# Performance work log

Measured on AMD Instinct MI355X. Metric: run time of the kernel, lower is better.

The kernel has to match this reference:

```python
import jax, jax.numpy as jnp
import numpy as np

B, N, V, E, T = 32, 256, 16, 1024, 5
MAX_N, ANNO, ND, VD, A_ACT = 256, 18, 64, 64, 3


def position_encoding_init(n_position, emb_dim):
    pe = np.array([[pos / np.power(10000, 2 * (j // 2) / emb_dim) for j in range(emb_dim)]
                   if pos != 0 else np.zeros(emb_dim) for pos in range(n_position)])
    pe[1:, 0::2] = np.sin(pe[1:, 0::2])
    pe[1:, 1::2] = np.cos(pe[1:, 1::2])
    return jnp.asarray(pe, jnp.float32)


def gru_cell(x, h, Wih, Whh, bih=None, bhh=None):
    # PyTorch GRUCell semantics. Wih: [3H, in], Whh: [3H, H]
    gi = x @ Wih.T + (bih if bih is not None else 0.0)
    gh = h @ Whh.T + (bhh if bhh is not None else 0.0)
    i_r, i_z, i_n = jnp.split(gi, 3, axis=1)
    h_r, h_z, h_n = jnp.split(gh, 3, axis=1)
    r = jax.nn.sigmoid(i_r + h_r)
    z = jax.nn.sigmoid(i_z + h_z)
    n = jnp.tanh(i_n + r * h_n)
    return (1.0 - z) * n + z * h


def setup_inputs() -> dict:
    key = jax.random.key(0)
    ks = jax.random.split(key, 20)
    dec_in = E + ND + 2 * VD
    inp = {
        "annotation": jax.random.normal(ks[0], (B, N, ANNO), jnp.float32),
        "A_out": jax.random.bernoulli(ks[1], 0.05, (B, N, N)).astype(jnp.float32),
        "A_in": jax.random.bernoulli(ks[2], 0.05, (B, N, N)).astype(jnp.float32),
        "from_node": jax.random.randint(ks[3], (B,), 0, MAX_N),
        "vnf_now": jax.random.uniform(ks[4], (B, V), jnp.float32),
        "vnf_all": jax.random.uniform(ks[5], (B, V), jnp.float32),
        "mask": jax.random.randint(ks[6], (B * N,), 0, 2),
        "anno_W": jax.random.normal(ks[7], (ANNO, E), jnp.float32),
        "gru_Wih": jax.random.normal(ks[8], (3 * E, 2 * E), jnp.float32) / np.sqrt(2 * E),
        "gru_Whh": jax.random.normal(ks[9], (3 * E, E), jnp.float32) / np.sqrt(E),
        "vnf_now_W": jax.random.normal(ks[10], (V, VD), jnp.float32),
        "vnf_all_W": jax.random.normal(ks[11], (V, VD), jnp.float32),
        "dgru_Wih": jax.random.normal(ks[12], (6 * E, dec_in), jnp.float32) / np.sqrt(dec_in),
        "dgru_Whh": jax.random.normal(ks[13], (6 * E, 2 * E), jnp.float32) / np.sqrt(2 * E),
        "dgru_bih": jax.random.normal(ks[14], (6 * E,), jnp.float32) * 0.01,
        "dgru_bhh": jax.random.normal(ks[15], (6 * E,), jnp.float32) * 0.01,
        "out_W1": jax.random.normal(ks[16], (E, 2 * E), jnp.float32) / np.sqrt(2 * E),
        "out_b1": jnp.zeros((E,), jnp.float32),
        "out_W2": jax.random.normal(ks[17], (A_ACT, E), jnp.float32) / np.sqrt(E),
        "out_b2": jnp.zeros((A_ACT,), jnp.float32),
        "pos_enc": position_encoding_init(MAX_N, ND),
    }
    return inp


def reference(annotation, A_out, A_in, from_node, vnf_now, vnf_all, mask,
              anno_W, gru_Wih, gru_Whh, vnf_now_W, vnf_all_W,
              dgru_Wih, dgru_Whh, dgru_bih, dgru_bhh,
              out_W1, out_b1, out_W2, out_b2, pos_enc):
    BN = B * N
    # ---- encoder (GG-NN): block-diagonal adjacency matmul == batched matmul ----
    h = annotation.reshape(BN, ANNO) @ anno_W  # [BN, E]

    def step(h, _):
        hb = h.reshape(B, N, E)
        a_out = jnp.einsum('bnm,bme->bne', A_out, hb).reshape(BN, E)
        a_in = jnp.einsum('bnm,bme->bne', A_in, hb).reshape(BN, E)
        a = jnp.concatenate([a_out, a_in], axis=1)  # [BN, 2E]
        return gru_cell(a, h, gru_Wih, gru_Whh), None

    enc_out, _ = jax.lax.scan(step, h, None, length=T)  # [BN, E]

    # ---- decoder step ----
    vn = (vnf_now @ vnf_now_W)[:, None, :]  # [B,1,VD] (repeat over N)
    va = (vnf_all @ vnf_all_W)[:, None, :]
    npos = pos_enc[from_node][:, None, :]   # [B,1,ND]
    vn = jnp.broadcast_to(vn, (B, N, VD)).reshape(BN, VD)
    va = jnp.broadcast_to(va, (B, N, VD)).reshape(BN, VD)
    npos = jnp.broadcast_to(npos, (B, N, ND)).reshape(BN, ND)

    concat_input = jnp.concatenate([enc_out, npos, va, vn], axis=1)
    h0 = jnp.zeros((BN, 2 * E), jnp.float32)
    hidden = gru_cell(concat_input, h0, dgru_Wih, dgru_Whh, dgru_bih, dgru_bhh)

    mid = jax.nn.relu(hidden @ out_W1.T + out_b1)
    output = (mid @ out_W2.T + out_b2).reshape(B, N, A_ACT)

    max_v = jnp.max(output, axis=(1, 2), keepdims=True)  # [B,1,1]
    output = output - (max_v + 1.0)
    mask_f = jnp.where(mask == 1, 1.0, 1e10).astype(jnp.float32).reshape(B, N, 1)
    output = mask_f * output + 1.0

    node_logits = output[:, :, 0]            # [B, N]
    vnf_logits = output[:, :, 1:]            # [B, N, 2]
    return node_logits, vnf_logits, hidden
```

## Files before the change

### kernel.cpp

```cpp
#include <hip/hip_runtime.h>
#include <hip/hip_bf16.h>
#include <math.h>

#define B_ 32
#define N_ 256
#define E_ 1024
#define BN_ 8192

typedef __hip_bfloat16 bf16;
typedef __bf16 bf8v __attribute__((ext_vector_type(8)));
typedef float  f4v  __attribute__((ext_vector_type(4)));

__device__ __forceinline__ float b2f(bf16 v) {
    unsigned short u = *(unsigned short*)&v;
    return __uint_as_float(((unsigned)u) << 16);
}
__device__ __forceinline__ unsigned short f2bu(float f) {
    bf16 h = __float2bfloat16(f);
    return *(unsigned short*)&h;
}
__device__ __forceinline__ float4 load4bf(const bf16* p) {
    ushort4 u = *(const ushort4*)p;
    return make_float4(__uint_as_float((unsigned)u.x << 16),
                       __uint_as_float((unsigned)u.y << 16),
                       __uint_as_float((unsigned)u.z << 16),
                       __uint_as_float((unsigned)u.w << 16));
}
__device__ __forceinline__ void store4bf(bf16* p, float a, float b, float c, float d) {
    ushort4 u = make_ushort4(f2bu(a), f2bu(b), f2bu(c), f2bu(d));
    *(ushort4*)p = u;
}
__device__ __forceinline__ float safe_sigm(float x) {
    x = fminf(fmaxf(x, -40.0f), 40.0f);
    return 1.0f / (1.0f + expf(-x));
}
__device__ __forceinline__ float safe_tanh(float x) {
    x = fminf(fmaxf(x, -15.0f), 15.0f);
    float t = expf(2.0f * x);
    return (t - 1.0f) / (t + 1.0f);
}
__device__ __forceinline__ void glds16(const bf16* g, bf16* l) {
    __builtin_amdgcn_global_load_lds(
        (__attribute__((address_space(1))) const void*)g,
        (__attribute__((address_space(3))) void*)l, 16, 0, 0);
}

#define MFMA16(d, a, b) d = __builtin_amdgcn_mfma_f32_16x16x32_bf16(a, b, d, 0, 0, 0)

__global__ __launch_bounds__(256)
void w2bf_kernel(const float* __restrict__ src, bf16* __restrict__ dst, int n4)
{
    int i = blockIdx.x * 256 + threadIdx.x;
    if (i < n4) {
        float4 v = ((const float4*)src)[i];
        store4bf(dst + (size_t)i * 4, v.x, v.y, v.z, v.w);
    }
}

__global__ __launch_bounds__(256)
void wgpack_kernel(const float* __restrict__ Wih, const float* __restrict__ Whh,
                   bf16* __restrict__ Wg)
{
    const int wr = blockIdx.x;
    const int e16 = wr / 48, rem = wr % 48;
    const int gate = rem >> 4, eL = rem & 15;
    const int e = e16 * 16 + eL;
    const float* s1 = Wih + (size_t)(gate * 1024 + e) * 2048;
    const float* s2 = Whh + (size_t)(gate * 1024 + e) * 1024;
    bf16* d = Wg + (size_t)wr * 3072;
    const int k0 = threadIdx.x * 4;
#pragma unroll
    for (int rep = 0; rep < 2; ++rep) {
        int k = k0 + rep * 1024;
        float4 v = *(const float4*)(s1 + k);
        store4bf(d + k, v.x, v.y, v.z, v.w);
    }
    {
        float4 v = *(const float4*)(s2 + k0);
        store4bf(d + 2048 + k0, v.x, v.y, v.z, v.w);
    }
}

__global__ __launch_bounds__(256)
void dgpack_kernel(const float* __restrict__ Wih, bf16* __restrict__ Wg)
{
    const int wr = blockIdx.x;
    const int e16 = wr / 48, rem = wr % 48;
    const int gate = rem >> 4, eL = rem & 15;
    const int e = e16 * 16 + eL;
    const float* s = Wih + (size_t)(gate * 2048 + e) * 1216;
    bf16* d = Wg + (size_t)wr * 1216;
    for (int k4 = threadIdx.x; k4 < 304; k4 += 256) {
        float4 v = *(const float4*)(s + k4 * 4);
        store4bf(d + k4 * 4, v.x, v.y, v.z, v.w);
    }
}

__global__ __launch_bounds__(256)
void anno_kernel(const float* __restrict__ anno, const float* __restrict__ W,
                 bf16* __restrict__ Hb)
{
    __shared__ float s[18];
    int row = blockIdx.x;
    if (threadIdx.x < 18) s[threadIdx.x] = anno[row * 18 + threadIdx.x];
    __syncthreads();
    for (int j = threadIdx.x; j < 1024; j += 256) {
        float acc = 0.0f;
#pragma unroll
        for (int k = 0; k < 18; ++k) acc = fmaf(s[k], W[k * 1024 + j], acc);
        Hb[(size_t)row * 1024 + j] = __float2bfloat16(acc);
    }
}

__global__ __launch_bounds__(256)
void bmm_kernel(const float* __restrict__ Aout, const float* __restrict__ Ain,
                const bf16* __restrict__ H, bf16* __restrict__ Abuf)
{
    __shared__ float As[16][68];
    __shared__ float Bs[16][68];
    const int z = blockIdx.z;
    const int b = z >> 1, which = z & 1;
    const float* Amat = (which ? Ain : Aout) + (size_t)b * N_ * N_;
    const bf16* Bmat = H + (size_t)b * N_ * E_;
    const int t = threadIdx.x;
    const int tx = t & 15, ty = t >> 4;
    const int bm = blockIdx.x * 64;
    const int bn = blockIdx.y * 64;
    const int ar = t >> 2, ak = (t & 3) << 2;
    const int kr = t >> 4, kn = (t & 15) << 2;
    float acc[4][4] = {};
    for (int k0 = 0; k0 < N_; k0 += 16) {
        float4 av = *(const float4*)(Amat + (size_t)(bm + ar) * N_ + k0 + ak);
        As[ak + 0][ar] = av.x; As[ak + 1][ar] = av.y;
        As[ak + 2][ar] = av.z; As[ak + 3][ar] = av.w;
        float4 bv = load4bf(Bmat + (size_t)(k0 + kr) * E_ + bn + kn);
        *(float4*)&Bs[kr][kn] = bv;
        __syncthreads();
#pragma unroll
        for (int kk = 0; kk < 16; ++kk) {
            float4 a4 = *(const float4*)&As[kk][ty << 2];
            float4 b4 = *(const float4*)&Bs[kk][tx << 2];
            float am[4] = {a4.x, a4.y, a4.z, a4.w};
            float bb[4] = {b4.x, b4.y, b4.z, b4.w};
#pragma unroll
            for (int i = 0; i < 4; ++i)
#pragma unroll
                for (int j = 0; j < 4; ++j)
                    acc[i][j] = fmaf(am[i], bb[j], acc[i][j]);
        }
        __syncthreads();
    }
#pragma unroll
    for (int i = 0; i < 4; ++i) {
        int row = b * N_ + bm + (ty << 2) + i;
        int col = which * 1024 + bn + (tx << 2);
        store4bf(&Abuf[(size_t)row * 2048 + col], acc[i][0], acc[i][1], acc[i][2], acc[i][3]);
    }
}

__global__ __launch_bounds__(256)
void htrans_kernel(const bf16* __restrict__ H, bf16* __restrict__ HbT)
{
    __shared__ float s[64][65];
    const int b = blockIdx.z;
    const int e0 = blockIdx.x * 64;
    const int n0 = blockIdx.y * 64;
    const bf16* Hb = H + (size_t)b * N_ * E_;
    bf16* Tb = HbT + (size_t)b * E_ * N_;
    const int t = threadIdx.x;
    const int tr = t >> 4, tc = (t & 15) << 2;
#pragma unroll
    for (int i = 0; i < 4; ++i) {
        float4 v = load4bf(Hb + (size_t)(n0 + tr + i * 16) * E_ + e0 + tc);
        s[tr + i * 16][tc + 0] = v.x; s[tr + i * 16][tc + 1] = v.y;
        s[tr + i * 16][tc + 2] = v.z; s[tr + i * 16][tc + 3] = v.w;
    }
    __syncthreads();
#pragma unroll
    for (int i = 0; i < 4; ++i) {
        int e = tr + i * 16;
        store4bf(Tb + (size_t)(e0 + e) * N_ + n0 + tc,
                 s[tc + 0][e], s[tc + 1][e], s[tc + 2][e], s[tc + 3][e]);
    }
}

__global__ __launch_bounds__(256)
void bmm_mfma_kernel(const bf16* __restrict__ Aoutb, const bf16* __restrict__ Ainb,
                     const bf16* __restrict__ HbT, bf16* __restrict__ Abuf)
{
    __shared__ bf16 As[64 * 32];
    __shared__ bf16 Bs[64 * 32];
    const int t = threadIdx.x;
    const int lane = t & 63, w = t >> 6;
    const int wm = (w >> 1) * 32, wn = (w & 1) * 32;
    const int z = blockIdx.z, b = z >> 1, which = z & 1;
    const int bm = blockIdx.x * 64, bn = blockIdx.y * 64;
    const int quad = lane >> 4, fr = lane & 15;
    const int srow = t >> 2, slot = t & 3;
    const int g = (slot + ((srow >> 1) & 3)) & 3;
    const int lds_off = srow * 32 + slot * 8;

    f4v acc[2][2];
#pragma unroll
    for (int i = 0; i < 2; ++i)
#pragma unroll
        for (int j = 0; j < 2; ++j) acc[i][j] = (f4v){0.f, 0.f, 0.f, 0.f};

    int aoff[2], boff[2];
#pragma unroll
    for (int i = 0; i < 2; ++i) {
        int arow = wm + 16 * i + fr;
        int s = (quad - ((arow >> 1) & 3)) & 3;
        aoff[i] = arow * 32 + s * 8;
    }
#pragma unroll
    for (int j = 0; j < 2; ++j) {
        int n = wn + 16 * j + fr;
        int s = (quad - ((n >> 1) & 3)) & 3;
        boff[j] = n * 32 + s * 8;
    }

    const bf16* Ap = (which ? Ainb : Aoutb) + (size_t)b * N_ * N_
                   + (size_t)(bm + srow) * N_ + g * 8;
    const bf16* Bp = HbT + (size_t)b * E_ * N_ + (size_t)(bn + srow) * N_ + g * 8;
    for (int k0 = 0; k0 < N_; k0 += 32) {
        float4 av = *(const float4*)(Ap + k0);
        float4 bv4 = *(const float4*)(Bp + k0);
        __syncthreads();
        *(float4*)(As + lds_off) = av;
        *(float4*)(Bs + lds_off) = bv4;
        __syncthreads();
        bf8v af0 = *(const bf8v*)(As + aoff[0]);
        bf8v af1 = *(const bf8v*)(As + aoff[1]);
#pragma unroll
        for (int j = 0; j < 2; ++j) {
            bf8v bv = *(const bf8v*)(Bs + boff[j]);
            MFMA16(acc[0][j], af0, bv);
            MFMA16(acc[1][j], af1, bv);
        }
    }
#pragma unroll
    for (int i = 0; i < 2; ++i)
#pragma unroll
        for (int j = 0; j < 2; ++j)
#pragma unroll
            for (int r = 0; r < 4; ++r) {
                int row = b * N_ + bm + wm + 16 * i + quad * 4 + r;
                int col = which * 1024 + bn + wn + 16 * j + fr;
                Abuf[(size_t)row * 2048 + col] = __float2bfloat16(acc[i][j][r]);
            }
}

__global__ __launch_bounds__(256, 2)
void enc_gru_kernel(const bf16* __restrict__ Aab, const bf16* __restrict__ Wg,
                    const bf16* __restrict__ Hcur, bf16* __restrict__ Hnext)
{
    __shared__ __align__(16) bf16 As[2 * 128 * 32];
    __shared__ __align__(16) bf16 Bs[2 * 192 * 32];
    const int t = threadIdx.x;
    const int lane = t & 63, w = t >> 6;
    const int wm = (w >> 1) * 64;
    const int wnH = (w & 1);
    const int bm = blockIdx.x * 128;
    const int bY = blockIdx.y;
    const int quad = lane >> 4, fr = lane & 15;

    f4v ar[2][4], az[2][4], ani[2][4], anh[2][4];
#pragma unroll
    for (int gq = 0; gq < 2; ++gq)
#pragma unroll
        for (int i = 0; i < 4; ++i) {
            ar[gq][i] = (f4v){0.f, 0.f, 0.f, 0.f};
            az[gq][i] = (f4v){0.f, 0.f, 0.f, 0.f};
            ani[gq][i] = (f4v){0.f, 0.f, 0.f, 0.f};
            anh[gq][i] = (f4v){0.f, 0.f, 0.f, 0.f};
        }

    int aoff[4];
#pragma unroll
    for (int i = 0; i < 4; ++i) {
        int row = wm + 16 * i + fr;
        int s = (quad - ((row >> 1) & 3)) & 3;
        aoff[i] = row * 32 + s * 8;
    }
    int boff[2][3];
#pragma unroll
    for (int gq = 0; gq < 2; ++gq)
#pragma unroll
        for (int gt = 0; gt < 3; ++gt) {
            int nb = wnH * 96 + gq * 48 + gt * 16 + fr;
            int s = (quad - ((nb >> 1) & 3)) & 3;
            boff[gq][gt] = nb * 32 + s * 8;
        }

    const int sr = lane >> 2, ss = lane & 3;
    const int lrA0 = w * 16 + sr;
    const int lrA1 = 64 + w * 16 + sr;
    const int gA0 = (ss + ((lrA0 >> 1) & 3)) & 3;
    const int gA1 = (ss + ((lrA1 >> 1) & 3)) & 3;
    const bf16* apA0 = Aab + (size_t)(bm + lrA0) * 2048 + gA0 * 8;
    const bf16* apA1 = Aab + (size_t)(bm + lrA1) * 2048 + gA1 * 8;
    const bf16* hpA0 = Hcur + (size_t)(bm + lrA0) * 1024 + gA0 * 8;
    const bf16* hpA1 = Hcur + (size_t)(bm + lrA1) * 1024 + gA1 * 8;
    const int lrB0 = w * 16 + sr, lrB1 = 64 + w * 16 + sr, lrB2 = 128 + w * 16 + sr;
    const int gB0 = (ss + ((lrB0 >> 1) & 3)) & 3;
    const int gB1 = (ss + ((lrB1 >> 1) & 3)) & 3;
    const int gB2 = (ss + ((lrB2 >> 1) & 3)) & 3;
    const bf16* bp0 = Wg + (size_t)(bY * 192 + lrB0) * 3072 + gB0 * 8;
    const bf16* bp1 = Wg + (size_t)(bY * 192 + lrB1) * 3072 + gB1 * 8;
    const bf16* bp2 = Wg + (size_t)(bY * 192 + lrB2) * 3072 + gB2 * 8;
    const int oA0 = (w * 16) * 32, oA1 = (64 + w * 16) * 32;
    const int oB0 = (w * 16) * 32, oB1 = (64 + w * 16) * 32, oB2 = (128 + w * 16) * 32;

#define ENC_STAGE(K, BUF) do {                                                 \
    const int k_ = (K);                                                        \
    const bf16* a0_ = (k_ < 2048) ? apA0 + k_ : hpA0 + (k_ - 2048);            \
    const bf16* a1_ = (k_ < 2048) ? apA1 + k_ : hpA1 + (k_ - 2048);            \
    glds16(a0_, As + (BUF) * 4096 + oA0);                                      \
    glds16(a1_, As + (BUF) * 4096 + oA1);                                      \
    glds16(bp0 + k_, Bs + (BUF) * 6144 + oB0);                                 \
    glds16(bp1 + k_, Bs + (BUF) * 6144 + oB1);                                 \
    glds16(bp2 + k_, Bs + (BUF) * 6144 + oB2);                                 \
} while (0)

#define ENC_STEP(Ab, Bb, AN) do {                                              \
    bf8v af0 = *(const bf8v*)((Ab) + aoff[0]);                                 \
    bf8v af1 = *(const bf8v*)((Ab) + aoff[1]);                                 \
    bf8v af2 = *(const bf8v*)((Ab) + aoff[2]);                                 \
    bf8v af3 = *(const bf8v*)((Ab) + aoff[3]);                                 \
    _Pragma("unroll")                                                          \
    for (int gq = 0; gq < 2; ++gq) {                                           \
        bf8v br_ = *(const bf8v*)((Bb) + boff[gq][0]);                         \
        bf8v bz_ = *(const bf8v*)((Bb) + boff[gq][1]);                         \
        bf8v bn_ = *(const bf8v*)((Bb) + boff[gq][2]);                         \
        MFMA16(ar[gq][0], af0, br_); MFMA16(ar[gq][1], af1, br_);              \
        MFMA16(ar[gq][2], af2, br_); MFMA16(ar[gq][3], af3, br_);              \
        MFMA16(az[gq][0], af0, bz_); MFMA16(az[gq][1], af1, bz_);              \
        MFMA16(az[gq][2], af2, bz_); MFMA16(az[gq][3], af3, bz_);              \
        MFMA16(AN[gq][0], af0, bn_); MFMA16(AN[gq][1], af1, bn_);              \
        MFMA16(AN[gq][2], af2, bn_); MFMA16(AN[gq][3], af3, bn_);              \
    }                                                                          \
} while (0)

    ENC_STAGE(0, 0);
    ENC_STAGE(32, 1);
    int cur = 0;
#pragma unroll 2
    for (int k0 = 0; k0 < 2048; k0 += 32) {
        asm volatile("s_waitcnt vmcnt(5)" ::: "memory");
        __builtin_amdgcn_s_barrier();
        ENC_STEP(As + cur * 4096, Bs + cur * 6144, ani);
        __builtin_amdgcn_s_barrier();
        ENC_STAGE(k0 + 64, cur);
        cur ^= 1;
    }
#pragma unroll 2
    for (int k0 = 2048; k0 < 3040; k0 += 32) {
        asm volatile("s_waitcnt vmcnt(5)" ::: "memory");
        __builtin_amdgcn_s_barrier();
        ENC_STEP(As + cur * 4096, Bs + cur * 6144, anh);
        __builtin_amdgcn_s_barrier();
        if (k0 + 64 < 3072) ENC_STAGE(k0 + 64, cur);
        cur ^= 1;
    }
    asm volatile("s_waitcnt vmcnt(0)" ::: "memory");
    __builtin_amdgcn_s_barrier();
    ENC_STEP(As + cur * 4096, Bs + cur * 6144, anh);

#pragma unroll
    for (int gq = 0; gq < 2; ++gq) {
        const int e = bY * 64 + wnH * 32 + gq * 16 + fr;
#pragma unroll
        for (int i = 0; i < 4; ++i) {
#pragma unroll
            for (int r = 0; r < 4; ++r) {
                const int row = bm + wm + 16 * i + quad * 4 + r;
                float hv = b2f(Hcur[(size_t)row * 1024 + e]);
                float rg = safe_sigm(ar[gq][i][r]);
                float zg = safe_sigm(az[gq][i][r]);
                float ng = safe_tanh(ani[gq][i][r] + rg * anh[gq][i][r]);
                Hnext[(size_t)row * 1024 + e] =
                    __float2bfloat16((1.0f - zg) * ng + zg * hv);
            }
        }
    }
#undef ENC_STEP
#undef ENC_STAGE
}

__global__ __launch_bounds__(256, 2)
void dec_gru_kernel(const bf16* __restrict__ Cc, const bf16* __restrict__ Wg,
                    const float* __restrict__ bih, const float* __restrict__ bhh,
                    float* __restrict__ hidden)
{
    __shared__ __align__(16) bf16 As[2 * 128 * 32];
    __shared__ __align__(16) bf16 Bs[2 * 192 * 32];
    const int t = threadIdx.x;
    const int lane = t & 63, w = t >> 6;
    const int wm = (w >> 1) * 64;
    const int wnH = (w & 1);
    const int bm = blockIdx.x * 128;
    const int bY = blockIdx.y;
    const int quad = lane >> 4, fr = lane & 15;

    f4v ag[3][2][4];
#pragma unroll
    for (int c = 0; c < 3; ++c)
#pragma unroll
        for (int gq = 0; gq < 2; ++gq)
#pragma unroll
            for (int i = 0; i < 4; ++i) ag[c][gq][i] = (f4v){0.f, 0.f, 0.f, 0.f};

    int aoff[4];
#pragma unroll
    for (int i = 0; i < 4; ++i) {
        int row = wm + 16 * i + fr;
        int s = (quad - ((row >> 1) & 3)) & 3;
        aoff[i] = row * 32 + s * 8;
    }
    int boff[2][3];
#pragma unroll
    for (int gq = 0; gq < 2; ++gq)
#pragma unroll
        for (int gt = 0; gt < 3; ++gt) {
            int nb = wnH * 96 + gq * 48 + gt * 16 + fr;
            int s = (quad - ((nb >> 1) & 3)) & 3;
            boff[gq][gt] = nb * 32 + s * 8;
        }

    const int sr = lane >> 2, ss = lane & 3;
    const int lrA0 = w * 16 + sr;
    const int lrA1 = 64 + w * 16 + sr;
    const int gA0 = (ss + ((lrA0 >> 1) & 3)) & 3;
    const int gA1 = (ss + ((lrA1 >> 1) & 3)) & 3;
    const bf16* apA0 = Cc + (size_t)(bm + lrA0) * 1216 + gA0 * 8;
    const bf16* apA1 = Cc + (size_t)(bm + lrA1) * 1216 + gA1 * 8;
    const int lrB0 = w * 16 + sr, lrB1 = 64 + w * 16 + sr, lrB2 = 128 + w * 16 + sr;
    const int gB0 = (ss + ((lrB0 >> 1) & 3)) & 3;
    const int gB1 = (ss + ((lrB1 >> 1) & 3)) & 3;
    const int gB2 = (ss + ((lrB2 >> 1) & 3)) & 3;
    const bf16* bp0 = Wg + (size_t)(bY * 192 + lrB0) * 1216 + gB0 * 8;
    const bf16* bp1 = Wg + (size_t)(bY * 192 + lrB1) * 1216 + gB1 * 8;
    const bf16* bp2 = Wg + (size_t)(bY * 192 + lrB2) * 1216 + gB2 * 8;
    const int oA0 = (w * 16) * 32, oA1 = (64 + w * 16) * 32;
    const int oB0 = (w * 16) * 32, oB1 = (64 + w * 16) * 32, oB2 = (128 + w * 16) * 32;

    glds16(apA0, As + oA0);
    glds16(apA1, As + oA1);
    glds16(bp0, Bs + oB0);
    glds16(bp1, Bs + oB1);
    glds16(bp2, Bs + oB2);
    __syncthreads();
    int cur = 0;
    for (int k0 = 0; k0 < 1216; k0 += 32) {
        const int nb = cur ^ 1;
        if (k0 + 32 < 1216) {
            glds16(apA0 + k0 + 32, As + nb * 4096 + oA0);
            glds16(apA1 + k0 + 32, As + nb * 4096 + oA1);
            glds16(bp0 + k0 + 32, Bs + nb * 6144 + oB0);
            glds16(bp1 + k0 + 32, Bs + nb * 6144 + oB1);
            glds16(bp2 + k0 + 32, Bs + nb * 6144 + oB2);
        }
        const bf16* Ab = As + cur * 4096;
        const bf16* Bb = Bs + cur * 6144;
        bf8v af0 = *(const bf8v*)(Ab + aoff[0]);
        bf8v af1 = *(const bf8v*)(Ab + aoff[1]);
        bf8v af2 = *(const bf8v*)(Ab + aoff[2]);
        bf8v af3 = *(const bf8v*)(Ab + aoff[3]);
#pragma unroll
        for (int gq = 0; gq < 2; ++gq) {
            bf8v br_ = *(const bf8v*)(Bb + boff[gq][0]);
            bf8v bz_ = *(const bf8v*)(Bb + boff[gq][1]);
            bf8v bn_ = *(const bf8v*)(Bb + boff[gq][2]);
            MFMA16(ag[0][gq][0], af0, br_); MFMA16(ag[0][gq][1], af1, br_);
            MFMA16(ag[0][gq][2], af2, br_); MFMA16(ag[0][gq][3], af3, br_);
            MFMA16(ag[1][gq][0], af0, bz_); MFMA16(ag[1][gq][1], af1, bz_);
            MFMA16(ag[1][gq][2], af2, bz_); MFMA16(ag[1][gq][3], af3, bz_);
            MFMA16(ag[2][gq][0], af0, bn_); MFMA16(ag[2][gq][1], af1, bn_);
            MFMA16(ag[2][gq][2], af2, bn_); MFMA16(ag[2][gq][3], af3, bn_);
        }
        __syncthreads();
        cur = nb;
    }

#pragma unroll
    for (int gq = 0; gq < 2; ++gq) {
        const int e = bY * 64 + wnH * 32 + gq * 16 + fr;
        const float br = bih[e] + bhh[e];
        const float bz = bih[2048 + e] + bhh[2048 + e];
        const float bni = bih[4096 + e];
        const float bnh = bhh[4096 + e];
#pragma unroll
        for (int i = 0; i < 4; ++i) {
#pragma unroll
            for (int r = 0; r < 4; ++r) {
                const int row = bm + wm + 16 * i + quad * 4 + r;
                float rr = safe_sigm(ag[0][gq][i][r] + br);
                float zz = safe_sigm(ag[1][gq][i][r] + bz);
                float nn = safe_tanh(ag[2][gq][i][r] + bni + rr * bnh);
                hidden[(size_t)row * 2048 + e] = (1.0f - zz) * nn;
            }
        }
    }
}

__global__ __launch_bounds__(128)
void vnva_kernel(const float* __restrict__ vnf_now, const float* __restrict__ vnf_all,
                 const float* __restrict__ Wn, const float* __restrict__ Wa,
                 float* __restrict__ vn, float* __restrict__ va)
{
    int b = blockIdx.x, t = threadIdx.x;
    if (t < 64) {
        float s = 0.f;
#pragma unroll
        for (int k = 0; k < 16; ++k) s = fmaf(vnf_now[b * 16 + k], Wn[k * 64 + t], s);
        vn[b * 64 + t] = s;
    } else {
        int d = t - 64;
        float s = 0.f;
#pragma unroll
        for (int k = 0; k < 16; ++k) s = fmaf(vnf_all[b * 16 + k], Wa[k * 64 + d], s);
        va[b * 64 + d] = s;
    }
}

__global__ __launch_bounds__(256)
void concat_kernel(const bf16* __restrict__ H, const float* __restrict__ pos_enc,
                   const int* __restrict__ from_node, const float* __restrict__ va,
                   const float* __restrict__ vn, bf16* __restrict__ Cc)
{
    int row = blockIdx.x;
    int b = row >> 8;
    int fn = from_node[b];
    const bf16* hsrc = H + (size_t)row * 1024;
    bf16* dst = Cc + (size_t)row * 1216;
    for (int c8 = threadIdx.x; c8 < 152; c8 += 256) {
        int c = c8 * 8;
        if (c < 1024) {
            *(uint4*)(dst + c) = *(const uint4*)(hsrc + c);
        } else {
#pragma unroll
            for (int j = 0; j < 8; ++j) {
                int col = c + j;
                float v;
                if (col < 1088)      v = pos_enc[fn * 64 + (col - 1024)];
                else if (col < 1152) v = va[b * 64 + (col - 1088)];
                else                 v = vn[b * 64 + (col - 1152)];
                dst[col] = __float2bfloat16(v);
            }
        }
    }
}

__global__ __launch_bounds__(256)
void out1_mfma_kernel(const float* __restrict__ H, const bf16* __restrict__ W1b,
                      const float* __restrict__ bias, bf16* __restrict__ mid)
{
    __shared__ bf16 As[64 * 32];
    __shared__ bf16 Ws[256 * 32];
    const int t = threadIdx.x;
    const int lane = t & 63, w = t >> 6;
    const int bm = blockIdx.x * 64, bn = blockIdx.y * 256;
    const int quad = lane >> 4, fr = lane & 15;
    const int srow = t >> 2, slot = t & 3;
    const int g = (slot + ((srow >> 1) & 3)) & 3;
    const int lds_off = srow * 32 + slot * 8;

    f4v acc[4][4];
#pragma unroll
    for (int i = 0; i < 4; ++i)
#pragma unroll
        for (int j = 0; j < 4; ++j) acc[i][j] = (f4v){0.f, 0.f, 0.f, 0.f};

    int aoff[4], boff[4];
#pragma unroll
    for (int i = 0; i < 4; ++i) {
        int arow = 16 * i + fr;
        int s = (quad - ((arow >> 1) & 3)) & 3;
        aoff[i] = arow * 32 + s * 8;
    }
#pragma unroll
    for (int j = 0; j < 4; ++j) {
        int n = w * 64 + 16 * j + fr;
        int s = (quad - ((n >> 1) & 3)) & 3;
        boff[j] = n * 32 + s * 8;
    }

    const float* Hp = H + (size_t)(bm + srow) * 2048 + g * 8;
    const bf16* Wp0 = W1b + (size_t)(bn + srow) * 2048 + g * 8;
    const bf16* Wp1 = W1b + (size_t)(bn + srow + 64) * 2048 + g * 8;
    const bf16* Wp2 = W1b + (size_t)(bn + srow + 128) * 2048 + g * 8;
    const bf16* Wp3 = W1b + (size_t)(bn + srow + 192) * 2048 + g * 8;

    for (int k0 = 0; k0 < 2048; k0 += 32) {
        float4 h0 = *(const float4*)(Hp + k0);
        float4 h1 = *(const float4*)(Hp + k0 + 4);
        float4 w0 = *(const float4*)(Wp0 + k0);
        float4 w1 = *(const float4*)(Wp1 + k0);
        float4 w2 = *(const float4*)(Wp2 + k0);
        float4 w3 = *(const float4*)(Wp3 + k0);
        uint4 pk;
        pk.x = (unsigned)f2bu(h0.x) | ((unsigned)f2bu(h0.y) << 16);
        pk.y = (unsigned)f2bu(h0.z) | ((unsigned)f2bu(h0.w) << 16);
        pk.z = (unsigned)f2bu(h1.x) | ((unsigned)f2bu(h1.y) << 16);
        pk.w = (unsigned)f2bu(h1.z) | ((unsigned)f2bu(h1.w) << 16);
        __syncthreads();
        *(uint4*)(As + lds_off) = pk;
        *(float4*)(Ws + lds_off) = w0;
        *(float4*)(Ws + 2048 + lds_off) = w1;
        *(float4*)(Ws + 4096 + lds_off) = w2;
        *(float4*)(Ws + 6144 + lds_off) = w3;
        __syncthreads();
        bf8v af0 = *(const bf8v*)(As + aoff[0]);
        bf8v af1 = *(const bf8v*)(As + aoff[1]);
        bf8v af2 = *(const bf8v*)(As + aoff[2]);
        bf8v af3 = *(const bf8v*)(As + aoff[3]);
#pragma unroll
        for (int j = 0; j < 4; ++j) {
            bf8v bv = *(const bf8v*)(Ws + boff[j]);
            MFMA16(acc[0][j], af0, bv);
            MFMA16(acc[1][j], af1, bv);
            MFMA16(acc[2][j], af2, bv);
            MFMA16(acc[3][j], af3, bv);
        }
    }
#pragma unroll
    for (int j = 0; j < 4; ++j) {
        const int col = bn + w * 64 + 16 * j + fr;
        const float bb = bias[col];
#pragma unroll
        for (int i = 0; i < 4; ++i) {
#pragma unroll
            for (int r = 0; r < 4; ++r) {
                const int row = bm + 16 * i + quad * 4 + r;
                mid[(size_t)row * 1024 + col] = __float2bfloat16(fmaxf(acc[i][j][r] + bb, 0.0f));
            }
        }
    }
}

__global__ __launch_bounds__(64)
void out2_kernel(const bf16* __restrict__ mid, const float* __restrict__ W2,
                 const float* __restrict__ b2, float* __restrict__ outb)
{
    int row = blockIdx.x, t = threadIdx.x;
    float s0 = 0.f, s1 = 0.f, s2 = 0.f;
    for (int k = t; k < 1024; k += 64) {
        float m = b2f(mid[(size_t)row * 1024 + k]);
        s0 = fmaf(m, W2[k], s0);
        s1 = fmaf(m, W2[1024 + k], s1);
        s2 = fmaf(m, W2[2048 + k], s2);
    }
#pragma unroll
    for (int off = 32; off > 0; off >>= 1) {
        s0 += __shfl_down(s0, off, 64);
        s1 += __shfl_down(s1, off, 64);
        s2 += __shfl_down(s2, off, 64);
    }
    if (t == 0) {
        outb[row * 3 + 0] = s0 + b2[0];
        outb[row * 3 + 1] = s1 + b2[1];
        outb[row * 3 + 2] = s2 + b2[2];
    }
}

__global__ __launch_bounds__(64)
void max_kernel(const float* __restrict__ outb, float* __restrict__ maxb)
{
    int b = blockIdx.x, t = threadIdx.x;
    float m = -3.0e38f;
    for (int i = t; i < 768; i += 64) m = fmaxf(m, outb[b * 768 + i]);
#pragma unroll
    for (int off = 32; off > 0; off >>= 1) m = fmaxf(m, __shfl_down(m, off, 64));
    if (t == 0) maxb[b] = m;
}

__global__ __launch_bounds__(256)
void mask_kernel(const float* __restrict__ outb, const float* __restrict__ maxb,
                 const int* __restrict__ mask, float* __restrict__ out)
{
    int idx = blockIdx.x * 256 + threadIdx.x;
    if (idx >= BN_ * 3) return;
    int row = idx / 3, c = idx - row * 3;
    int b = row >> 8;
    float v = outb[idx] - (maxb[b] + 1.0f);
    float mf = (mask[row] == 1) ? 1.0f : 1e10f;
    v = mf * v + 1.0f;
    if (c == 0) out[row] = v;
    else        out[8192 + row * 2 + (c - 1)] = v;
}

extern "C" void kernel_launch(void* const* d_in, const int* in_sizes, int n_in,
                              void* d_out, int out_size, void* d_ws, size_t ws_size,
                              hipStream_t stream)
{
    const float* annotation = (const float*)d_in[0];
    const float* A_out      = (const float*)d_in[1];
    const float* A_in       = (const float*)d_in[2];
    const int*   from_node  = (const int*)d_in[3];
    const float* vnf_now    = (const float*)d_in[4];
    const float* vnf_all    = (const float*)d_in[5];
    const int*   mask       = (const int*)d_in[6];
    const float* anno_W     = (const float*)d_in[7];
    const float* gru_Wih    = (const float*)d_in[8];
    const float* gru_Whh    = (const float*)d_in[9];
    const float* vnf_now_W  = (const float*)d_in[10];
    const float* vnf_all_W  = (const float*)d_in[11];
    const float* dgru_Wih   = (const float*)d_in[12];
    const float* dgru_bih   = (const float*)d_in[14];
    const float* dgru_bhh   = (const float*)d_in[15];
    const float* out_W1     = (const float*)d_in[16];
    const float* out_b1     = (const float*)d_in[17];
    const float* out_W2     = (const float*)d_in[18];
    const float* out_b2     = (const float*)d_in[19];
    const float* pos_enc    = (const float*)d_in[20];
    float* out = (float*)d_out;

    bf16*  Abuf = (bf16*)d_ws;
    bf16*  Wenc = Abuf + (size_t)8192 * 2048;
    bf16*  Wg   = Wenc;
    bf16*  WgD  = Wenc;
    bf16*  W1b  = Wenc;
    float* fbuf = (float*)(Wenc + (size_t)9437184);
    float* vnb  = fbuf;
    float* vab  = vnb + 2048;
    float* outb = vab + 2048;
    float* maxb = outb + 24576;
    bf16*  Aoutb = (bf16*)(maxb + 32);
    bf16*  Ainb  = Aoutb + (size_t)32 * 256 * 256;
    bf16*  HbT   = Ainb + (size_t)32 * 256 * 256;

    const size_t NEED_FULL = (size_t)(16777216 + 9437184) * 2 + 28704 * 4
                           + (size_t)(4194304 + 8388608) * 2;
    const bool full = ws_size >= NEED_FULL;

    float* hidden = out + 24576;
    bf16* Hb0 = (bf16*)hidden;
    bf16* Hb1 = Hb0 + (size_t)8192 * 1024;
    bf16* Cc  = Abuf;
    bf16* mid = Abuf;

    wgpack_kernel<<<3072, 256, 0, stream>>>(gru_Wih, gru_Whh, Wg);
    if (full) {
        w2bf_kernel<<<2048, 256, 0, stream>>>(A_out, Aoutb, 32 * 256 * 256 / 4);
        w2bf_kernel<<<2048, 256, 0, stream>>>(A_in,  Ainb,  32 * 256 * 256 / 4);
    }

    anno_kernel<<<8192, 256, 0, stream>>>(annotation, anno_W, Hb0);

    const bf16* hc = Hb0;
    bf16* hn = Hb1;
    for (int s = 0; s < 5; ++s) {
        if (full) {
            htrans_kernel<<<dim3(16, 4, 32), 256, 0, stream>>>(hc, HbT);
            bmm_mfma_kernel<<<dim3(4, 16, 64), 256, 0, stream>>>(Aoutb, Ainb, HbT, Abuf);
        } else {
            bmm_kernel<<<dim3(4, 16, 64), 256, 0, stream>>>(A_out, A_in, hc, Abuf);
        }
        enc_gru_kernel<<<dim3(64, 16), 256, 0, stream>>>(Abuf, Wg, hc, hn);
        bf16* tmp = (bf16*)hc; hc = hn; hn = tmp;
    }

    vnva_kernel<<<32, 128, 0, stream>>>(vnf_now, vnf_all, vnf_now_W, vnf_all_W, vnb, vab);
    concat_kernel<<<8192, 256, 0, stream>>>(hc, pos_enc, from_node, vab, vnb, Cc);

    dgpack_kernel<<<6144, 256, 0, stream>>>(dgru_Wih, WgD);
    dec_gru_kernel<<<dim3(64, 32), 256, 0, stream>>>(Cc, WgD, dgru_bih, dgru_bhh, hidden);

    w2bf_kernel<<<2048, 256, 0, stream>>>(out_W1, W1b, 1024 * 2048 / 4);
    out1_mfma_kernel<<<dim3(128, 4), 256, 0, stream>>>(hidden, W1b, out_b1, mid);

    out2_kernel<<<8192, 64, 0, stream>>>(mid, out_W2, out_b2, outb);
    max_kernel<<<32, 64, 0, stream>>>(outb, maxb);
    mask_kernel<<<96, 256, 0, stream>>>(outb, maxb, mask, out);
}
```

Baseline: 1.512 ms.

## Triple-buffer encoder GRU GEMM pipeline and swizzle block order for cache reuse

The encoder GRU GEMM goes from a double-buffered LDS pipeline to a triple-buffered one. That keeps two K-tiles of loads in flight (vmcnt 10) while the current tile is computed, and the loop is now fully unrolled by three with an explicit tail. The 2D grid becomes a 1D grid of 1024 blocks remapped so that groups of 8 column blocks share consecutive row blocks, aiming to improve L2 reuse of the weight and activation tiles. The cost is more LDS per block (about 61KB), which could limit occupancy, and extra code size.

Measured after the change: 3.747 ms. 148% more time.

```diff
diff --git a/kernel.cpp b/kernel.cpp
--- a/kernel.cpp
+++ b/kernel.cpp
@@ -255,14 +255,15 @@
 void enc_gru_kernel(const bf16* __restrict__ Aab, const bf16* __restrict__ Wg,
                     const bf16* __restrict__ Hcur, bf16* __restrict__ Hnext)
 {
-    __shared__ __align__(16) bf16 As[2 * 128 * 32];
-    __shared__ __align__(16) bf16 Bs[2 * 192 * 32];
+    __shared__ __align__(16) bf16 As[3 * 128 * 32];
+    __shared__ __align__(16) bf16 Bs[3 * 192 * 32];
     const int t = threadIdx.x;
     const int lane = t & 63, w = t >> 6;
     const int wm = (w >> 1) * 64;
     const int wnH = (w & 1);
-    const int bm = blockIdx.x * 128;
-    const int bY = blockIdx.y;
+    const int id = blockIdx.x;
+    const int bm = ((id >> 3) & 63) * 128;
+    const int bY = (id & 7) + 8 * (id >> 9);
     const int quad = lane >> 4, fr = lane & 15;
 
     f4v ar[2][4], az[2][4], ani[2][4], anh[2][4];
@@ -342,30 +343,25 @@
     }                                                                          \
 } while (0)
 
+#define ENC_PIPE(KK, BUF, WAIT) do {                                           \
+    asm volatile("s_waitcnt vmcnt(" #WAIT ")" ::: "memory");                   \
+    __builtin_amdgcn_s_barrier();                                              \
+    if ((KK) < 2048) { ENC_STEP(As + (BUF) * 4096, Bs + (BUF) * 6144, ani); }  \
+    else             { ENC_STEP(As + (BUF) * 4096, Bs + (BUF) * 6144, anh); }  \
+    __builtin_amdgcn_s_barrier();                                              \
+} while (0)
+
     ENC_STAGE(0, 0);
     ENC_STAGE(32, 1);
-    int cur = 0;
-#pragma unroll 2
-    for (int k0 = 0; k0 < 2048; k0 += 32) {
-        asm volatile("s_waitcnt vmcnt(5)" ::: "memory");
-        __builtin_amdgcn_s_barrier();
-        ENC_STEP(As + cur * 4096, Bs + cur * 6144, ani);
-        __builtin_amdgcn_s_barrier();
-        ENC_STAGE(k0 + 64, cur);
-        cur ^= 1;
-    }
-#pragma unroll 2
-    for (int k0 = 2048; k0 < 3040; k0 += 32) {
-        asm volatile("s_waitcnt vmcnt(5)" ::: "memory");
-        __builtin_amdgcn_s_barrier();
-        ENC_STEP(As + cur * 4096, Bs + cur * 6144, anh);
-        __builtin_amdgcn_s_barrier();
-        if (k0 + 64 < 3072) ENC_STAGE(k0 + 64, cur);
-        cur ^= 1;
-    }
-    asm volatile("s_waitcnt vmcnt(0)" ::: "memory");
-    __builtin_amdgcn_s_barrier();
-    ENC_STEP(As + cur * 4096, Bs + cur * 6144, anh);
+    ENC_STAGE(64, 2);
+    for (int k0 = 0; k0 < 2976; k0 += 96) {
+        ENC_PIPE(k0, 0, 10);      ENC_STAGE(k0 + 96, 0);
+        ENC_PIPE(k0 + 32, 1, 10); ENC_STAGE(k0 + 128, 1);
+        ENC_PIPE(k0 + 64, 2, 10); ENC_STAGE(k0 + 160, 2);
+    }
+    ENC_PIPE(2976, 0, 10);
+    ENC_PIPE(3008, 1, 5);
+    ENC_PIPE(3040, 2, 0);
 
 #pragma unroll
     for (int gq = 0; gq < 2; ++gq) {
@@ -384,6 +380,7 @@
             }
         }
     }
+#undef ENC_PIPE
 #undef ENC_STEP
 #undef ENC_STAGE
 }
@@ -757,7 +754,7 @@
         } else {
             bmm_kernel<<<dim3(4, 16, 64), 256, 0, stream>>>(A_out, A_in, hc, Abuf);
         }
-        enc_gru_kernel<<<dim3(64, 16), 256, 0, stream>>>(Abuf, Wg, hc, hn);
+        enc_gru_kernel<<<1024, 256, 0, stream>>>(Abuf, Wg, hc, hn);
         bf16* tmp = (bf16*)hc; hc = hn; hn = tmp;
     }
 
```
